# Kernel tuning notes

Hardware: AMD Instinct MI355X
Metric: run time of the kernel (lower is better)

Reference implementation:

```python
import jax, jax.numpy as jnp
import numpy as np

N = 4096
TOPK = 16
LEAKY = 0.2
LN_EPS = 1e-5


def _gat(x, W, a_s, a_d, b, src, dst, heads):
    # PyG-style GATConv (self-loops already included in src/dst).
    n = x.shape[0]
    h = (x @ W).reshape(n, heads, -1)                      # [N,H,F]
    e = jax.nn.leaky_relu((h * a_s).sum(-1)[src] + (h * a_d).sum(-1)[dst], LEAKY)  # [E,H]
    m = jax.ops.segment_max(e, dst, num_segments=n)        # segment softmax over dst
    p = jnp.exp(e - m[dst])
    s = jax.ops.segment_sum(p, dst, num_segments=n)
    alpha = p / s[dst]                                     # [E,H]
    out = jax.ops.segment_sum(alpha[:, :, None] * h[src], dst, num_segments=n)  # [N,H,F]
    return out.reshape(n, -1) + b


def _ln(x, g, b):
    mu = x.mean(-1, keepdims=True)
    v = ((x - mu) ** 2).mean(-1, keepdims=True)
    return (x - mu) / jnp.sqrt(v + LN_EPS) * g + b


def _transformer_layer(x, wqkv, bqkv, wo, bo, g1, b1g, w1, bb1, w2, bb2, g2, b2g, nhead):
    n, d = x.shape
    dh = d // nhead
    qkv = x @ wqkv.T + bqkv                                # [N,3d]
    q, k, v = jnp.split(qkv, 3, axis=-1)
    q = q.reshape(n, nhead, dh)
    k = k.reshape(n, nhead, dh)
    v = v.reshape(n, nhead, dh)
    scores = jnp.einsum('nhd,mhd->hnm', q, k) / jnp.sqrt(jnp.float32(dh))
    attn = jax.nn.softmax(scores, axis=-1)
    o = jnp.einsum('hnm,mhd->nhd', attn, v).reshape(n, d)
    x = _ln(x + (o @ wo.T + bo), g1, b1g)
    ff = jax.nn.relu(x @ w1 + bb1) @ w2 + bb2
    return _ln(x + ff, g2, b2g)


def _learn_graph(window, gl_w, gl_b):
    h = jnp.tanh(window @ gl_w + gl_b)                     # [N,hid]
    sim = h @ h.T                                          # [N,N]
    adj = jax.nn.relu(sim)
    masked = jnp.where(jnp.eye(N, dtype=bool), -1e9, adj)  # exclude self in top-k
    _, idx = jax.lax.top_k(masked, TOPK)                   # [N,TOPK]
    src = idx.reshape(-1)
    dst = jnp.repeat(jnp.arange(N), TOPK)
    loop = jnp.arange(N)
    return jnp.concatenate([src, loop]), jnp.concatenate([dst, loop])


def setup_inputs() -> dict:
    key = jax.random.key(0)
    ks = iter(jax.random.split(key, 64))
    def rn(shape, s=0.05):
        return jax.random.normal(next(ks), shape, jnp.float32) * s
    d = dict(
        window=rn((N, 256), 1.0),
        gl_w=rn((256, 256)), gl_b=rn((256,)),
        enc_W=rn((3, 256, 256)), enc_asrc=rn((3, 4, 64)), enc_adst=rn((3, 4, 64)), enc_b=rn((3, 256)),
        tr_wqkv=rn((2, 768, 256)), tr_bqkv=rn((2, 768)),
        tr_wo=rn((2, 256, 256)), tr_bo=rn((2, 256)),
        tr_ln1_g=jnp.ones((2, 256), jnp.float32), tr_ln1_b=jnp.zeros((2, 256), jnp.float32),
        tr_w1=rn((2, 256, 512)), tr_b1=rn((2, 512)),
        tr_w2=rn((2, 512, 256)), tr_b2=rn((2, 256)),
        tr_ln2_g=jnp.ones((2, 256), jnp.float32), tr_ln2_b=jnp.zeros((2, 256), jnp.float32),
        skip_w=rn((256, 256)), skip_b=rn((256,)),
        dec_W=rn((2, 256, 256)), dec_asrc=rn((2, 4, 64)), dec_adst=rn((2, 4, 64)), dec_b=rn((2, 256)),
        dec_lW=rn((256, 256)), dec_lasrc=rn((1, 1, 256)), dec_ladst=rn((1, 1, 256)), dec_lb=rn((256,)),
    )
    return d


def reference(window, gl_w, gl_b, enc_W, enc_asrc, enc_adst, enc_b,
              tr_wqkv, tr_bqkv, tr_wo, tr_bo, tr_ln1_g, tr_ln1_b,
              tr_w1, tr_b1, tr_w2, tr_b2, tr_ln2_g, tr_ln2_b,
              skip_w, skip_b, dec_W, dec_asrc, dec_adst, dec_b,
              dec_lW, dec_lasrc, dec_ladst, dec_lb):
    src, dst = _learn_graph(window, gl_w, gl_b)
    # encoder: 3 GAT layers with ReLU
    x = window
    for i in range(3):
        x = jax.nn.relu(_gat(x, enc_W[i], enc_asrc[i], enc_adst[i], enc_b[i], src, dst, 4))
    # transformer bottleneck (batch of 1 sequence of N tokens)
    h = x
    for i in range(2):
        h = _transformer_layer(h, tr_wqkv[i], tr_bqkv[i], tr_wo[i], tr_bo[i],
                               tr_ln1_g[i], tr_ln1_b[i], tr_w1[i], tr_b1[i],
                               tr_w2[i], tr_b2[i], tr_ln2_g[i], tr_ln2_b[i], 4)
    # skip connection
    h = h + (window @ skip_w + skip_b)
    # decoder: 2 GAT layers with ReLU, then single-head GAT
    x = h
    for i in range(2):
        x = jax.nn.relu(_gat(x, dec_W[i], dec_asrc[i], dec_adst[i], dec_b[i], src, dst, 4))
    out = _gat(x, dec_lW, dec_lasrc[0], dec_ladst[0], dec_lb, src, dst, 1)
    return out.T
```

## Files before the change

kernel.cpp:

```cpp
#include <hip/hip_runtime.h>
#include <math.h>

#define NN 4096
#define DM 256

enum { ACT_NONE = 0, ACT_RELU = 1, ACT_TANH = 2 };

typedef __attribute__((ext_vector_type(8))) short short8v;
typedef __attribute__((ext_vector_type(16))) float f32x16;

__device__ __forceinline__ unsigned short f2bf(float f) {
  unsigned int u = __float_as_uint(f);
  unsigned int r = (u + 0x7FFFu + ((u >> 16) & 1u)) >> 16;
  return (unsigned short)r;
}
__device__ __forceinline__ float bf2f(unsigned short u) {
  return __uint_as_float(((unsigned int)u) << 16);
}

struct CastJob { const float* s; unsigned short* d; int n4; };
__global__ __launch_bounds__(256) void castall_k(CastJob j0, CastJob j1, CastJob j2) {
  const CastJob* jp = (blockIdx.y == 0) ? &j0 : (blockIdx.y == 1) ? &j1 : &j2;
  const int i = blockIdx.x * 256 + threadIdx.x;
  if (i < jp->n4) {
    const float4 v = ((const float4*)jp->s)[i];
    ushort4 u;
    u.x = f2bf(v.x); u.y = f2bf(v.y); u.z = f2bf(v.z); u.w = f2bf(v.w);
    ((ushort4*)jp->d)[i] = u;
  }
}

struct TJob { const float* s; unsigned short* d; int K; int N; };
struct TJobs { TJob j[11]; };
__global__ __launch_bounds__(256) void tcastall_k(TJobs js) {
  const TJob jb = js.j[blockIdx.z];
  const int n0 = blockIdx.x * 32, k0 = blockIdx.y * 32;
  if (n0 >= jb.N || k0 >= jb.K) return;
  __shared__ float tile[32][33];
  const int tx = threadIdx.x & 31, ty = threadIdx.x >> 5;
#pragma unroll
  for (int r2 = 0; r2 < 4; r2++)
    tile[ty + r2 * 8][tx] = jb.s[(size_t)(k0 + ty + r2 * 8) * jb.N + n0 + tx];
  __syncthreads();
#pragma unroll
  for (int r2 = 0; r2 < 4; r2++)
    jb.d[(size_t)(n0 + ty + r2 * 8) * jb.K + k0 + tx] = f2bf(tile[tx][ty + r2 * 8]);
}

__global__ __launch_bounds__(256) void split_k(
    const float* __restrict__ h, unsigned short* __restrict__ Aext,
    unsigned short* __restrict__ Bext) {
  const int n = blockIdx.x, t = threadIdx.x;
  const float v = h[(size_t)n * DM + t];
  const unsigned short hi = f2bf(v);
  const unsigned short lo = f2bf(v - bf2f(hi));
  unsigned short* ar = Aext + (size_t)n * 768;
  unsigned short* br = Bext + (size_t)n * 768;
  ar[t] = hi; ar[256 + t] = lo; ar[512 + t] = hi;
  br[t] = hi; br[256 + t] = hi; br[512 + t] = lo;
}

template<bool BT, int ACT, bool BIAS, bool RES>
__global__ __launch_bounds__(256) void gemm_k(
    const float* __restrict__ A, const float* __restrict__ B,
    const float* __restrict__ bias, const float* __restrict__ res,
    float* __restrict__ C, int M, int N, int K) {
  __shared__ float As[16][64];
  __shared__ float Bs[16][64];
  const int t = threadIdx.x;
  const int tx = t & 15, ty = t >> 4;
  const int m0 = blockIdx.y * 64, n0 = blockIdx.x * 64;
  float acc[4][4];
#pragma unroll
  for (int i = 0; i < 4; i++)
#pragma unroll
    for (int j = 0; j < 4; j++) acc[i][j] = 0.f;

  const int i_ld = t >> 2, kq = t & 3;
  for (int k0 = 0; k0 < K; k0 += 16) {
    float4 a4 = *(const float4*)(A + (size_t)(m0 + i_ld) * K + k0 + kq * 4);
    As[kq * 4 + 0][i_ld] = a4.x; As[kq * 4 + 1][i_ld] = a4.y;
    As[kq * 4 + 2][i_ld] = a4.z; As[kq * 4 + 3][i_ld] = a4.w;
    if (BT) {
      float4 b4 = *(const float4*)(B + (size_t)(n0 + i_ld) * K + k0 + kq * 4);
      Bs[kq * 4 + 0][i_ld] = b4.x; Bs[kq * 4 + 1][i_ld] = b4.y;
      Bs[kq * 4 + 2][i_ld] = b4.z; Bs[kq * 4 + 3][i_ld] = b4.w;
    } else {
      const int kk = t >> 4, j4 = (t & 15) * 4;
      float4 b4 = *(const float4*)(B + (size_t)(k0 + kk) * N + n0 + j4);
      *(float4*)&Bs[kk][j4] = b4;
    }
    __syncthreads();
#pragma unroll
    for (int kk = 0; kk < 16; kk++) {
      const float4 av = *(const float4*)&As[kk][ty * 4];
      const float4 bv = *(const float4*)&Bs[kk][tx * 4];
      acc[0][0] += av.x * bv.x; acc[0][1] += av.x * bv.y;
      acc[0][2] += av.x * bv.z; acc[0][3] += av.x * bv.w;
      acc[1][0] += av.y * bv.x; acc[1][1] += av.y * bv.y;
      acc[1][2] += av.y * bv.z; acc[1][3] += av.y * bv.w;
      acc[2][0] += av.z * bv.x; acc[2][1] += av.z * bv.y;
      acc[2][2] += av.z * bv.z; acc[2][3] += av.z * bv.w;
      acc[3][0] += av.w * bv.x; acc[3][1] += av.w * bv.y;
      acc[3][2] += av.w * bv.z; acc[3][3] += av.w * bv.w;
    }
    __syncthreads();
  }
  const int n = n0 + tx * 4;
#pragma unroll
  for (int i = 0; i < 4; i++) {
    const int m = m0 + ty * 4 + i;
    float4 v = make_float4(acc[i][0], acc[i][1], acc[i][2], acc[i][3]);
    if (BIAS) {
      v.x += bias[n + 0]; v.y += bias[n + 1];
      v.z += bias[n + 2]; v.w += bias[n + 3];
    }
    if (RES) {
      const float4 rv = *(const float4*)(res + (size_t)m * N + n);
      v.x += rv.x; v.y += rv.y; v.z += rv.z; v.w += rv.w;
    }
    if (ACT == ACT_RELU) {
      v.x = fmaxf(v.x, 0.f); v.y = fmaxf(v.y, 0.f);
      v.z = fmaxf(v.z, 0.f); v.w = fmaxf(v.w, 0.f);
    } else if (ACT == ACT_TANH) {
      v.x = tanhf(v.x); v.y = tanhf(v.y); v.z = tanhf(v.z); v.w = tanhf(v.w);
    }
    *(float4*)(C + (size_t)m * N + n) = v;
  }
}

template<int ACT, bool BIAS, bool RES, bool F32OUT, bool B16OUT>
__global__ __launch_bounds__(256) void mgemm_k(
    const unsigned short* __restrict__ A, const unsigned short* __restrict__ Bt,
    const float* __restrict__ bias, const float* __restrict__ res,
    float* __restrict__ C, unsigned short* __restrict__ Cb,
    int M, int N, int K) {
  __shared__ short As[64][64];
  __shared__ short Bs[64][64];
  const int t = threadIdx.x;
  const int m0 = blockIdx.y * 64, n0 = blockIdx.x * 64;
  const int wid = t >> 6, l = t & 63, l31 = l & 31, g = l >> 5;
  const int wm = wid >> 1, wn = wid & 1;
  f32x16 acc;
#pragma unroll
  for (int r = 0; r < 16; r++) acc[r] = 0.f;

  const int r0 = wid * 16;
  const int lrow = l >> 3;
  const int pos = l & 7;
  const int swz = (pos ^ lrow) << 3;

  for (int k0 = 0; k0 < K; k0 += 64) {
#pragma unroll
    for (int j = 0; j < 2; j++) {
      const int row = r0 + j * 8 + lrow;
      const short* ga = (const short*)A + (size_t)(m0 + row) * K + k0 + swz;
      const short* gb = (const short*)Bt + (size_t)(n0 + row) * K + k0 + swz;
      __builtin_amdgcn_global_load_lds(
          (const __attribute__((address_space(1))) unsigned int*)ga,
          (__attribute__((address_space(3))) unsigned int*)&As[r0 + j * 8][0],
          16, 0, 0);
      __builtin_amdgcn_global_load_lds(
          (const __attribute__((address_space(1))) unsigned int*)gb,
          (__attribute__((address_space(3))) unsigned int*)&Bs[r0 + j * 8][0],
          16, 0, 0);
    }
    __syncthreads();
#pragma unroll
    for (int ck = 0; ck < 4; ck++) {
      const int c = ck * 2 + g;
      const short8v af = *(const short8v*)&As[wm * 32 + l31][(c ^ (l31 & 7)) * 8];
      const short8v bf = *(const short8v*)&Bs[wn * 32 + l31][(c ^ (l31 & 7)) * 8];
      acc = __builtin_amdgcn_mfma_f32_32x32x16_bf16(bf, af, acc, 0, 0, 0);
    }
    __syncthreads();
  }
  const int m = m0 + wm * 32 + l31;
#pragma unroll
  for (int b = 0; b < 4; b++) {
    const int n = n0 + wn * 32 + b * 8 + g * 4;
    float4 v = make_float4(acc[b * 4 + 0], acc[b * 4 + 1],
                           acc[b * 4 + 2], acc[b * 4 + 3]);
    if (BIAS) {
      v.x += bias[n + 0]; v.y += bias[n + 1];
      v.z += bias[n + 2]; v.w += bias[n + 3];
    }
    if (RES) {
      const float4 rv = *(const float4*)(res + (size_t)m * N + n);
      v.x += rv.x; v.y += rv.y; v.z += rv.z; v.w += rv.w;
    }
    if (ACT == ACT_RELU) {
      v.x = fmaxf(v.x, 0.f); v.y = fmaxf(v.y, 0.f);
      v.z = fmaxf(v.z, 0.f); v.w = fmaxf(v.w, 0.f);
    }
    if (F32OUT) *(float4*)(C + (size_t)m * N + n) = v;
    if (B16OUT) {
      ushort4 uv;
      uv.x = f2bf(v.x); uv.y = f2bf(v.y); uv.z = f2bf(v.z); uv.w = f2bf(v.w);
      *(ushort4*)(Cb + (size_t)m * N + n) = uv;
    }
  }
}

__global__ __launch_bounds__(256) void topk16_k(
    const float* __restrict__ sim, int* __restrict__ idxo, int rowbase) {
  const int r = blockIdx.x, t = threadIdx.x;
  const int grow = rowbase + r;
  float val[16];
#pragma unroll
  for (int q = 0; q < 16; q++) {
    const int jj = q * 256 + t;
    float v = sim[(size_t)r * NN + jj];
    v = fmaxf(v, 0.f);
    if (jj == grow) v = -1.f;
    val[q] = v;
  }
  __shared__ float cv[64];
  __shared__ int cjs[64];
  const int wave = t >> 6, lane = t & 63;
  float myv = -3.f; int myj = 0;
  for (int it = 0; it < 16; it++) {
    float bv = -10.f; int bj = 0;
#pragma unroll
    for (int q = 0; q < 16; q++)
      if (val[q] > bv) { bv = val[q]; bj = q * 256 + t; }
#pragma unroll
    for (int off = 1; off < 64; off <<= 1) {
      const float ov = __shfl_xor(bv, off);
      const int oj = __shfl_xor(bj, off);
      if (ov > bv || (ov == bv && oj < bj)) { bv = ov; bj = oj; }
    }
    if (lane == it) { myv = bv; myj = bj; }
    if ((bj & 255) == t) {
      const int q = bj >> 8;
#pragma unroll
      for (int qq = 0; qq < 16; qq++) if (qq == q) val[qq] = -2.f;
    }
  }
  if (lane < 16) { cv[wave * 16 + lane] = myv; cjs[wave * 16 + lane] = myj; }
  __syncthreads();
  if (wave == 0) {
    float bv2 = cv[lane]; int bj2 = cjs[lane];
    for (int it = 0; it < 16; it++) {
      float wv = bv2; int wj = bj2;
#pragma unroll
      for (int off = 1; off < 64; off <<= 1) {
        const float ov = __shfl_xor(wv, off);
        const int oj = __shfl_xor(wj, off);
        if (ov > wv || (ov == wv && oj < wj)) { wv = ov; wj = oj; }
      }
      if (lane == 0) idxo[(size_t)grow * 16 + it] = wj;
      if (wj == bj2) bv2 = -3.f;
    }
  }
}

template<int H>
__global__ __launch_bounds__(256) void gat_prep_k(
    const float* __restrict__ h, const float* __restrict__ as,
    const float* __restrict__ ad, float* __restrict__ es, float* __restrict__ ed) {
  __shared__ float bs[4], bd[4];
  const int n = blockIdx.x, t = threadIdx.x;
  const float v = h[(size_t)n * DM + t];
  float ps = v * as[t];
  float pd = v * ad[t];
#pragma unroll
  for (int off = 32; off >= 1; off >>= 1) {
    ps += __shfl_down(ps, off, 64);
    pd += __shfl_down(pd, off, 64);
  }
  const int wave = t >> 6, lane = t & 63;
  if (H == 4) {
    if (lane == 0) { es[n * 4 + wave] = ps; ed[n * 4 + wave] = pd; }
  } else {
    if (lane == 0) { bs[wave] = ps; bd[wave] = pd; }
    __syncthreads();
    if (t == 0) {
      es[n] = bs[0] + bs[1] + bs[2] + bs[3];
      ed[n] = bd[0] + bd[1] + bd[2] + bd[3];
    }
  }
}

template<int H, bool RELU, bool B16OUT>
__global__ __launch_bounds__(256) void gat_aggr_k(
    const float* __restrict__ h, const float* __restrict__ es,
    const float* __restrict__ ed, const int* __restrict__ idx,
    const float* __restrict__ bias, float* __restrict__ out,
    unsigned short* __restrict__ outb) {
  const int j = blockIdx.x, t = threadIdx.x;
  const int hd = (H == 4) ? (t >> 6) : 0;
  __shared__ int srcs[17];
  if (t < 16) srcs[t] = idx[(size_t)j * 16 + t];
  if (t == 16) srcs[16] = j;
  __syncthreads();
  const float edj = ed[j * H + hd];
  float e[17]; float m = -1e30f;
#pragma unroll
  for (int k = 0; k < 17; k++) {
    float ev = es[srcs[k] * H + hd] + edj;
    ev = (ev >= 0.f) ? ev : 0.2f * ev;
    e[k] = ev; m = fmaxf(m, ev);
  }
  float s = 0.f;
#pragma unroll
  for (int k = 0; k < 17; k++) { e[k] = expf(e[k] - m); s += e[k]; }
  const float inv = 1.f / s;
  float acc = 0.f;
#pragma unroll
  for (int k = 0; k < 17; k++) acc += e[k] * h[(size_t)srcs[k] * DM + t];
  acc = acc * inv + bias[t];
  if (RELU) acc = fmaxf(acc, 0.f);
  out[(size_t)j * DM + t] = acc;
  if (B16OUT) outb[(size_t)j * DM + t] = f2bf(acc);
}

__global__ __launch_bounds__(256) void kvfrag_k(
    const short* __restrict__ qkvs, short* __restrict__ kf,
    short* __restrict__ vf) {
  const int kc = blockIdx.x;
  const int h = blockIdx.y;
  const int t = threadIdx.x;
  __shared__ short Ks[32][72];
  __shared__ short Vs[32][72];
  {
    const int row = t >> 3, ch = t & 7;
    const short* kp = qkvs + (size_t)(kc * 32 + row) * 768 + 256 + h * 64 + ch * 8;
    *(short8v*)&Ks[row][ch * 8] = *(const short8v*)kp;
    const short* vp = qkvs + (size_t)(kc * 32 + row) * 768 + 512 + h * 64 + ch * 8;
    *(short8v*)&Vs[row][ch * 8] = *(const short8v*)vp;
  }
  __syncthreads();
  {
    const int dc = t >> 6, l = t & 63, l31 = l & 31, g = l >> 5;
    short8v kv;
#pragma unroll
    for (int e = 0; e < 8; e++) kv[e] = Ks[l31][dc * 16 + g * 8 + e];
    *(short8v*)(kf + ((size_t)(h * 128 + kc) * 4 + dc) * 512 + l * 8) = kv;
  }
  {
    const int db = t >> 7, kg = (t >> 6) & 1, l = t & 63, l31 = l & 31, g = l >> 5;
    short8v vv;
#pragma unroll
    for (int e = 0; e < 8; e++) {
      const int j = kg * 16 + g * 8 + e;
      const int jp = (j & 19) | ((j & 4) << 1) | ((j & 8) >> 1);
      vv[e] = Vs[jp][db * 32 + l31];
    }
    *(short8v*)(vf + (((size_t)(h * 128 + kc) * 2 + db) * 2 + kg) * 512 + l * 8) = vv;
  }
}

#define LOADKV(KF, VF, KC) do {                                               \
    const short* kp_ = kfrag + ((size_t)(KC)) * 2048 + l * 8;                 \
    KF##0 = *(const short8v*)(kp_);                                           \
    KF##1 = *(const short8v*)(kp_ + 512);                                     \
    KF##2 = *(const short8v*)(kp_ + 1024);                                    \
    KF##3 = *(const short8v*)(kp_ + 1536);                                    \
    const short* vp_ = vfrag + ((size_t)(KC)) * 2048 + l * 8;                 \
    VF##0 = *(const short8v*)(vp_);                                           \
    VF##1 = *(const short8v*)(vp_ + 512);                                     \
    VF##2 = *(const short8v*)(vp_ + 1024);                                    \
    VF##3 = *(const short8v*)(vp_ + 1536);                                    \
  } while (0)

#define PROCESS(KF, VF) do {                                                  \
    f32x16 accS;                                                              \
    _Pragma("unroll") for (int r = 0; r < 16; r++) accS[r] = 0.f;             \
    __builtin_amdgcn_s_setprio(1);                                            \
    accS = __builtin_amdgcn_mfma_f32_32x32x16_bf16(KF##0, qf[0], accS, 0, 0, 0); \
    accS = __builtin_amdgcn_mfma_f32_32x32x16_bf16(KF##1, qf[1], accS, 0, 0, 0); \
    accS = __builtin_amdgcn_mfma_f32_32x32x16_bf16(KF##2, qf[2], accS, 0, 0, 0); \
    accS = __builtin_amdgcn_mfma_f32_32x32x16_bf16(KF##3, qf[3], accS, 0, 0, 0); \
    __builtin_amdgcn_s_setprio(0);                                            \
    float mt = -1e30f;                                                        \
    _Pragma("unroll") for (int r = 0; r < 16; r++) mt = fmaxf(mt, accS[r]);   \
    mt = fmaxf(mt, __shfl_xor(mt, 32));                                       \
    float pv[16]; float ls = 0.f;                                             \
    if (__all(mt <= mrun + 11.5416f)) {                                       \
      _Pragma("unroll") for (int r = 0; r < 16; r++) {                        \
        pv[r] = exp2f(accS[r] - mrun); ls += pv[r];                           \
      }                                                                       \
      ls += __shfl_xor(ls, 32); lrun += ls;                                   \
    } else {                                                                  \
      const float mnew = fmaxf(mrun, mt);                                     \
      const float corr = exp2f(mrun - mnew);                                  \
      _Pragma("unroll") for (int r = 0; r < 16; r++) {                        \
        pv[r] = exp2f(accS[r] - mnew); ls += pv[r];                           \
      }                                                                       \
      ls += __shfl_xor(ls, 32);                                               \
      lrun = lrun * corr + ls; mrun = mnew;                                   \
      _Pragma("unroll") for (int r = 0; r < 16; r++) {                        \
        accO[0][r] *= corr; accO[1][r] *= corr;                               \
      }                                                                       \
    }                                                                         \
    union { unsigned int u[8]; short8v s[2]; } pf;                            \
    _Pragma("unroll") for (int r = 0; r < 8; r++) {                           \
      unsigned int po;                                                        \
      asm("v_cvt_pk_bf16_f32 %0, %1, %2"                                      \
          : "=v"(po) : "v"(pv[2 * r]), "v"(pv[2 * r + 1]));                   \
      pf.u[r] = po;                                                           \
    }                                                                         \
    __builtin_amdgcn_s_setprio(1);                                            \
    accO[0] = __builtin_amdgcn_mfma_f32_32x32x16_bf16(VF##0, pf.s[0], accO[0], 0, 0, 0); \
    accO[0] = __builtin_amdgcn_mfma_f32_32x32x16_bf16(VF##1, pf.s[1], accO[0], 0, 0, 0); \
    accO[1] = __builtin_amdgcn_mfma_f32_32x32x16_bf16(VF##2, pf.s[0], accO[1], 0, 0, 0); \
    accO[1] = __builtin_amdgcn_mfma_f32_32x32x16_bf16(VF##3, pf.s[1], accO[1], 0, 0, 0); \
    __builtin_amdgcn_s_setprio(0);                                            \
  } while (0)

__global__ __launch_bounds__(256) void attn_flash_k(
    const short* __restrict__ qkvs, const short* __restrict__ kfb,
    const short* __restrict__ vfb, unsigned short* __restrict__ opart,
    float* __restrict__ ml) {
  const int t = threadIdx.x;
  const int wv = t >> 6;
  const int l = t & 63;
  const int qb = (blockIdx.x * 4 + wv) * 32;
  const int h = blockIdx.y;
  const int z = blockIdx.z;
  const int l31 = l & 31, g = l >> 5;

  short8v qf[4];
  {
    const short* qp = qkvs + (size_t)(qb + l31) * 768 + h * 64 + g * 8;
#pragma unroll
    for (int c = 0; c < 4; c++) {
      short8v qv = *(const short8v*)(qp + c * 16);
#pragma unroll
      for (int e = 0; e < 8; e++)
        qv[e] = (short)f2bf(bf2f((unsigned short)qv[e]) * 0.18033688f);
      qf[c] = qv;
    }
  }

  f32x16 accO[2];
#pragma unroll
  for (int r = 0; r < 16; r++) { accO[0][r] = 0.f; accO[1][r] = 0.f; }
  float mrun = -1e30f, lrun = 0.f;

  const short* kfrag = kfb + (size_t)h * 128 * 2048;
  const short* vfrag = vfb + (size_t)h * 128 * 2048;
  const int kc0 = z * 32;

  short8v kA0, kA1, kA2, kA3, vA0, vA1, vA2, vA3;
  short8v kB0, kB1, kB2, kB3, vB0, vB1, vB2, vB3;
  LOADKV(kA, vA, kc0);
  for (int it = 0; it < 16; it++) {
    LOADKV(kB, vB, kc0 + (it * 2 + 1));
    PROCESS(kA, vA);
    LOADKV(kA, vA, kc0 + ((it * 2 + 2) & 31));
    PROCESS(kB, vB);
  }

  const int q = qb + l31;
  unsigned short* op = opart + ((size_t)z * NN + q) * DM + h * 64;
#pragma unroll
  for (int db = 0; db < 2; db++) {
#pragma unroll
    for (int rq = 0; rq < 4; rq++) {
      ushort4 v4;
      v4.x = f2bf(accO[db][rq * 4 + 0]);
      v4.y = f2bf(accO[db][rq * 4 + 1]);
      v4.z = f2bf(accO[db][rq * 4 + 2]);
      v4.w = f2bf(accO[db][rq * 4 + 3]);
      *(ushort4*)(op + db * 32 + rq * 8 + g * 4) = v4;
    }
  }
  if (g == 0) {
    ml[(((size_t)z * 4 + h) * NN + q) * 2 + 0] = mrun;
    ml[(((size_t)z * 4 + h) * NN + q) * 2 + 1] = lrun;
  }
}

__global__ __launch_bounds__(256) void attn_merge_k(
    const unsigned short* __restrict__ opart, const float* __restrict__ ml,
    unsigned short* __restrict__ ob) {
  const int q = blockIdx.x;
  const int t = threadIdx.x;
  const int h = t >> 6;
  float m[4], lv[4];
#pragma unroll
  for (int z = 0; z < 4; z++) {
    m[z]  = ml[(((size_t)z * 4 + h) * NN + q) * 2 + 0];
    lv[z] = ml[(((size_t)z * 4 + h) * NN + q) * 2 + 1];
  }
  const float ms = fmaxf(fmaxf(m[0], m[1]), fmaxf(m[2], m[3]));
  float w[4]; float ls = 0.f;
#pragma unroll
  for (int z = 0; z < 4; z++) {
    w[z] = exp2f(m[z] - ms);
    ls += lv[z] * w[z];
  }
  const float inv = 1.f / ls;
  float acc = 0.f;
#pragma unroll
  for (int z = 0; z < 4; z++)
    acc += bf2f(opart[((size_t)z * NN + q) * DM + t]) * w[z];
  ob[(size_t)q * DM + t] = f2bf(acc * inv);
}

__global__ __launch_bounds__(256) void ln_k(
    const float* __restrict__ x, const float* __restrict__ g,
    const float* __restrict__ b, float* __restrict__ y,
    unsigned short* __restrict__ yb) {
  __shared__ float bs[4], bs2[4];
  const int n = blockIdx.x, t = threadIdx.x;
  const float v = x[(size_t)n * DM + t];
  float s = v, s2 = v * v;
#pragma unroll
  for (int off = 32; off >= 1; off >>= 1) {
    s += __shfl_down(s, off, 64);
    s2 += __shfl_down(s2, off, 64);
  }
  const int wave = t >> 6, lane = t & 63;
  if (lane == 0) { bs[wave] = s; bs2[wave] = s2; }
  __syncthreads();
  const float ts = bs[0] + bs[1] + bs[2] + bs[3];
  const float ts2 = bs2[0] + bs2[1] + bs2[2] + bs2[3];
  const float mu = ts * (1.f / 256.f);
  const float var = ts2 * (1.f / 256.f) - mu * mu;
  const float rstd = 1.f / sqrtf(var + 1e-5f);
  const float o = (v - mu) * rstd * g[t] + b[t];
  y[(size_t)n * DM + t] = o;
  yb[(size_t)n * DM + t] = f2bf(o);
}

__global__ __launch_bounds__(1024) void transpose_k(
    const float* __restrict__ x, float* __restrict__ out) {
  __shared__ float tile[32][33];
  const int n0 = blockIdx.x * 32, c0 = blockIdx.y * 32;
  const int tx = threadIdx.x, ty = threadIdx.y;
  tile[ty][tx] = x[(size_t)(n0 + ty) * DM + c0 + tx];
  __syncthreads();
  out[(size_t)(c0 + ty) * NN + n0 + tx] = tile[tx][ty];
}

extern "C" void kernel_launch(void* const* d_in, const int* in_sizes, int n_in,
                              void* d_out, int out_size, void* d_ws, size_t ws_size,
                              hipStream_t stream) {
  (void)in_sizes; (void)n_in; (void)out_size; (void)ws_size;
  const float* window   = (const float*)d_in[0];
  const float* gl_w     = (const float*)d_in[1];
  const float* gl_b     = (const float*)d_in[2];
  const float* enc_W    = (const float*)d_in[3];
  const float* enc_asrc = (const float*)d_in[4];
  const float* enc_adst = (const float*)d_in[5];
  const float* enc_b    = (const float*)d_in[6];
  const float* tr_wqkv  = (const float*)d_in[7];
  const float* tr_bqkv  = (const float*)d_in[8];
  const float* tr_wo    = (const float*)d_in[9];
  const float* tr_bo    = (const float*)d_in[10];
  const float* tr_ln1_g = (const float*)d_in[11];
  const float* tr_ln1_b = (const float*)d_in[12];
  const float* tr_w1    = (const float*)d_in[13];
  const float* tr_b1    = (const float*)d_in[14];
  const float* tr_w2    = (const float*)d_in[15];
  const float* tr_b2    = (const float*)d_in[16];
  const float* tr_ln2_g = (const float*)d_in[17];
  const float* tr_ln2_b = (const float*)d_in[18];
  const float* skip_w   = (const float*)d_in[19];
  const float* skip_b   = (const float*)d_in[20];
  const float* dec_W    = (const float*)d_in[21];
  const float* dec_asrc = (const float*)d_in[22];
  const float* dec_adst = (const float*)d_in[23];
  const float* dec_b    = (const float*)d_in[24];
  const float* dec_lW   = (const float*)d_in[25];
  const float* dec_lasrc= (const float*)d_in[26];
  const float* dec_ladst= (const float*)d_in[27];
  const float* dec_lb   = (const float*)d_in[28];
  float* outp = (float*)d_out;

  float* ws   = (float*)d_ws;
  float* xa   = ws;
  float* xb   = ws + 1048576;
  float* hp   = ws + 2097152;
  float* t1   = ws + 3145728;
  float* hgl  = t1;
  float* mlb  = t1;
  float* qkvb = ws + 4194304;
  float* Rg   = ws + 6291456;
  float* simc = Rg;
  unsigned short* opartb = (unsigned short*)Rg;
  unsigned short* ffb    = (unsigned short*)Rg;
  float* es   = ws + 8388608;
  float* ed   = ws + 8404992;
  int*   idx  = (int*)(ws + 8421376);
  unsigned short* winb = (unsigned short*)(ws + 8486912);
  unsigned short* actb = (unsigned short*)(ws + 9011200);
  unsigned short* wb   = (unsigned short*)(ws + 9535488);

  unsigned short* encWt = wb;
  unsigned short* wqkvb = wb + 196608;
  unsigned short* wob   = wb + 589824;
  unsigned short* w1t   = wb + 720896;
  unsigned short* w2t   = wb + 983040;
  unsigned short* skipt = wb + 1245184;
  unsigned short* dect  = wb + 1310720;
  unsigned short* declt = wb + 1441792;

  unsigned short* Aext = (unsigned short*)qkvb;
  unsigned short* Bext = (unsigned short*)xa;

  short* kfb = (short*)hp;
  short* vfb = (short*)hp + 1048576;

  const dim3 B256(256);

  {
    CastJob c0{window, winb, 262144};
    CastJob c1{tr_wqkv, wqkvb, 98304};
    CastJob c2{tr_wo, wob, 32768};
    castall_k<<<dim3(1024, 3), B256, 0, stream>>>(c0, c1, c2);
    TJobs tj;
    for (int i = 0; i < 3; i++) tj.j[i] = {enc_W + (size_t)i * 65536, encWt + (size_t)i * 65536, 256, 256};
    for (int i = 0; i < 2; i++) tj.j[3 + i] = {tr_w1 + (size_t)i * 131072, w1t + (size_t)i * 131072, 256, 512};
    for (int i = 0; i < 2; i++) tj.j[5 + i] = {tr_w2 + (size_t)i * 131072, w2t + (size_t)i * 131072, 512, 256};
    tj.j[7] = {skip_w, skipt, 256, 256};
    for (int i = 0; i < 2; i++) tj.j[8 + i] = {dec_W + (size_t)i * 65536, dect + (size_t)i * 65536, 256, 256};
    tj.j[10] = {dec_lW, declt, 256, 256};
    tcastall_k<<<dim3(16, 16, 11), B256, 0, stream>>>(tj);
  }

  gemm_k<false, ACT_TANH, true, false><<<dim3(DM / 64, NN / 64), B256, 0, stream>>>(
      window, gl_w, gl_b, nullptr, hgl, NN, DM, DM);

  split_k<<<dim3(NN), B256, 0, stream>>>(hgl, Aext, Bext);
  for (int c = 0; c < 8; c++) {
    mgemm_k<ACT_NONE, false, false, true, false><<<dim3(64, 8), B256, 0, stream>>>(
        Aext + (size_t)c * 512 * 768, Bext, nullptr, nullptr, simc, nullptr,
        512, NN, 768);
    topk16_k<<<dim3(512), B256, 0, stream>>>(simc, idx, c * 512);
  }

  for (int i = 0; i < 3; i++) {
    const unsigned short* ain = (i == 0) ? winb : actb;
    mgemm_k<ACT_NONE, false, false, true, false><<<dim3(4, 64), B256, 0, stream>>>(
        ain, encWt + (size_t)i * 65536, nullptr, nullptr, hp, nullptr, NN, DM, DM);
    gat_prep_k<4><<<dim3(NN), B256, 0, stream>>>(hp, enc_asrc + i * 256, enc_adst + i * 256, es, ed);
    gat_aggr_k<4, true, true><<<dim3(NN), B256, 0, stream>>>(
        hp, es, ed, idx, enc_b + i * 256, xa, actb);
  }

  for (int i = 0; i < 2; i++) {
    mgemm_k<ACT_NONE, true, false, false, true><<<dim3(12, 64), B256, 0, stream>>>(
        actb, wqkvb + (size_t)i * 196608, tr_bqkv + i * 768, nullptr,
        nullptr, (unsigned short*)qkvb, NN, 768, DM);
    kvfrag_k<<<dim3(128, 4), B256, 0, stream>>>((const short*)qkvb, kfb, vfb);
    attn_flash_k<<<dim3(NN / 128, 4, 4), B256, 0, stream>>>(
        (const short*)qkvb, kfb, vfb, opartb, mlb);
    attn_merge_k<<<dim3(NN), B256, 0, stream>>>(opartb, mlb, actb);
    mgemm_k<ACT_NONE, true, true, true, false><<<dim3(4, 64), B256, 0, stream>>>(
        actb, wob + (size_t)i * 65536, tr_bo + i * 256, xa, t1, nullptr, NN, DM, DM);
    ln_k<<<dim3(NN), B256, 0, stream>>>(t1, tr_ln1_g + i * 256, tr_ln1_b + i * 256, xb, actb);
    mgemm_k<ACT_RELU, true, false, false, true><<<dim3(8, 64), B256, 0, stream>>>(
        actb, w1t + (size_t)i * 131072, tr_b1 + i * 512, nullptr,
        nullptr, ffb, NN, 512, DM);
    mgemm_k<ACT_NONE, true, true, true, false><<<dim3(4, 64), B256, 0, stream>>>(
        ffb, w2t + (size_t)i * 131072, tr_b2 + i * 256, xb, t1, nullptr, NN, DM, 512);
    ln_k<<<dim3(NN), B256, 0, stream>>>(t1, tr_ln2_g + i * 256, tr_ln2_b + i * 256, xa, actb);
  }

  mgemm_k<ACT_NONE, true, true, false, true><<<dim3(4, 64), B256, 0, stream>>>(
      winb, skipt, skip_b, xa, nullptr, actb, NN, DM, DM);

  mgemm_k<ACT_NONE, false, false, true, false><<<dim3(4, 64), B256, 0, stream>>>(
      actb, dect, nullptr, nullptr, hp, nullptr, NN, DM, DM);
  gat_prep_k<4><<<dim3(NN), B256, 0, stream>>>(hp, dec_asrc, dec_adst, es, ed);
  gat_aggr_k<4, true, true><<<dim3(NN), B256, 0, stream>>>(hp, es, ed, idx, dec_b, xb, actb);

  mgemm_k<ACT_NONE, false, false, true, false><<<dim3(4, 64), B256, 0, stream>>>(
      actb, dect + 65536, nullptr, nullptr, hp, nullptr, NN, DM, DM);
  gat_prep_k<4><<<dim3(NN), B256, 0, stream>>>(hp, dec_asrc + 256, dec_adst + 256, es, ed);
  gat_aggr_k<4, true, true><<<dim3(NN), B256, 0, stream>>>(hp, es, ed, idx, dec_b + 256, xb, actb);

  mgemm_k<ACT_NONE, false, false, true, false><<<dim3(4, 64), B256, 0, stream>>>(
      actb, declt, nullptr, nullptr, hp, nullptr, NN, DM, DM);
  gat_prep_k<1><<<dim3(NN), B256, 0, stream>>>(hp, dec_lasrc, dec_ladst, es, ed);
  gat_aggr_k<1, false, false><<<dim3(NN), B256, 0, stream>>>(hp, es, ed, idx, dec_lb, xa, nullptr);

  transpose_k<<<dim3(NN / 32, DM / 32), dim3(32, 32), 0, stream>>>(xa, outp);
}
```

Baseline: 693.9 us.

## Move graph-learning GEMM to split-bf16 MFMA and fuse tanh with hi/lo split

The fp32 SIMT GEMM for tanh(window@gl_w+b) is replaced by a split-bf16 (hi/lo, 3-term) MFMA GEMM. Its epilogue applies bias and tanh and writes the extended hi/lo operands for the similarity GEMM directly, which removes the separate split kernel and the fp32 intermediate round trip. The similarity GEMM also moves to a new kernel with 64x128 tiles and two accumulators per wave, so A fragments are reused across more columns. The cost is extra split/transpose kernels on window and gl_w, and a precision change in the tanh input from fp32 to a 3-term bf16 emulation.

```diff
diff --git a/kernel.cpp b/kernel.cpp
--- a/kernel.cpp
+++ b/kernel.cpp
@@ -47,85 +47,33 @@
     jb.d[(size_t)(n0 + ty + r2 * 8) * jb.K + k0 + tx] = f2bf(tile[tx][ty + r2 * 8]);
 }
 
-__global__ __launch_bounds__(256) void split_k(
-    const float* __restrict__ h, unsigned short* __restrict__ Aext,
-    unsigned short* __restrict__ Bext) {
+__global__ __launch_bounds__(256) void wsplit_k(
+    const float* __restrict__ w, unsigned short* __restrict__ Awin) {
   const int n = blockIdx.x, t = threadIdx.x;
-  const float v = h[(size_t)n * DM + t];
+  const float v = w[(size_t)n * DM + t];
   const unsigned short hi = f2bf(v);
   const unsigned short lo = f2bf(v - bf2f(hi));
-  unsigned short* ar = Aext + (size_t)n * 768;
-  unsigned short* br = Bext + (size_t)n * 768;
+  unsigned short* ar = Awin + (size_t)n * 768;
   ar[t] = hi; ar[256 + t] = lo; ar[512 + t] = hi;
-  br[t] = hi; br[256 + t] = hi; br[512 + t] = lo;
-}
-
-template<bool BT, int ACT, bool BIAS, bool RES>
-__global__ __launch_bounds__(256) void gemm_k(
-    const float* __restrict__ A, const float* __restrict__ B,
-    const float* __restrict__ bias, const float* __restrict__ res,
-    float* __restrict__ C, int M, int N, int K) {
-  __shared__ float As[16][64];
-  __shared__ float Bs[16][64];
-  const int t = threadIdx.x;
-  const int tx = t & 15, ty = t >> 4;
-  const int m0 = blockIdx.y * 64, n0 = blockIdx.x * 64;
-  float acc[4][4];
-#pragma unroll
-  for (int i = 0; i < 4; i++)
-#pragma unroll
-    for (int j = 0; j < 4; j++) acc[i][j] = 0.f;
-
-  const int i_ld = t >> 2, kq = t & 3;
-  for (int k0 = 0; k0 < K; k0 += 16) {
-    float4 a4 = *(const float4*)(A + (size_t)(m0 + i_ld) * K + k0 + kq * 4);
-    As[kq * 4 + 0][i_ld] = a4.x; As[kq * 4 + 1][i_ld] = a4.y;
-    As[kq * 4 + 2][i_ld] = a4.z; As[kq * 4 + 3][i_ld] = a4.w;
-    if (BT) {
-      float4 b4 = *(const float4*)(B + (size_t)(n0 + i_ld) * K + k0 + kq * 4);
-      Bs[kq * 4 + 0][i_ld] = b4.x; Bs[kq * 4 + 1][i_ld] = b4.y;
-      Bs[kq * 4 + 2][i_ld] = b4.z; Bs[kq * 4 + 3][i_ld] = b4.w;
-    } else {
-      const int kk = t >> 4, j4 = (t & 15) * 4;
-      float4 b4 = *(const float4*)(B + (size_t)(k0 + kk) * N + n0 + j4);
-      *(float4*)&Bs[kk][j4] = b4;
-    }
-    __syncthreads();
-#pragma unroll
-    for (int kk = 0; kk < 16; kk++) {
-      const float4 av = *(const float4*)&As[kk][ty * 4];
-      const float4 bv = *(const float4*)&Bs[kk][tx * 4];
-      acc[0][0] += av.x * bv.x; acc[0][1] += av.x * bv.y;
-      acc[0][2] += av.x * bv.z; acc[0][3] += av.x * bv.w;
-      acc[1][0] += av.y * bv.x; acc[1][1] += av.y * bv.y;
-      acc[1][2] += av.y * bv.z; acc[1][3] += av.y * bv.w;
-      acc[2][0] += av.z * bv.x; acc[2][1] += av.z * bv.y;
-      acc[2][2] += av.z * bv.z; acc[2][3] += av.z * bv.w;
-      acc[3][0] += av.w * bv.x; acc[3][1] += av.w * bv.y;
-      acc[3][2] += av.w * bv.z; acc[3][3] += av.w * bv.w;
-    }
-    __syncthreads();
-  }
-  const int n = n0 + tx * 4;
-#pragma unroll
-  for (int i = 0; i < 4; i++) {
-    const int m = m0 + ty * 4 + i;
-    float4 v = make_float4(acc[i][0], acc[i][1], acc[i][2], acc[i][3]);
-    if (BIAS) {
-      v.x += bias[n + 0]; v.y += bias[n + 1];
-      v.z += bias[n + 2]; v.w += bias[n + 3];
-    }
-    if (RES) {
-      const float4 rv = *(const float4*)(res + (size_t)m * N + n);
-      v.x += rv.x; v.y += rv.y; v.z += rv.z; v.w += rv.w;
-    }
-    if (ACT == ACT_RELU) {
-      v.x = fmaxf(v.x, 0.f); v.y = fmaxf(v.y, 0.f);
-      v.z = fmaxf(v.z, 0.f); v.w = fmaxf(v.w, 0.f);
-    } else if (ACT == ACT_TANH) {
-      v.x = tanhf(v.x); v.y = tanhf(v.y); v.z = tanhf(v.z); v.w = tanhf(v.w);
-    }
-    *(float4*)(C + (size_t)m * N + n) = v;
+}
+
+__global__ __launch_bounds__(256) void gsplit_k(
+    const float* __restrict__ g, unsigned short* __restrict__ Bgl) {
+  __shared__ float tile[32][33];
+  const int d0 = blockIdx.x * 32, k0 = blockIdx.y * 32;
+  const int tx = threadIdx.x & 31, ty = threadIdx.x >> 5;
+#pragma unroll
+  for (int r2 = 0; r2 < 4; r2++)
+    tile[ty + r2 * 8][tx] = g[(size_t)(k0 + ty + r2 * 8) * DM + d0 + tx];
+  __syncthreads();
+#pragma unroll
+  for (int r2 = 0; r2 < 4; r2++) {
+    const int d = d0 + ty + r2 * 8, k = k0 + tx;
+    const float v = tile[tx][ty + r2 * 8];
+    const unsigned short hi = f2bf(v);
+    const unsigned short lo = f2bf(v - bf2f(hi));
+    unsigned short* br = Bgl + (size_t)d * 768;
+    br[k] = hi; br[256 + k] = hi; br[512 + k] = lo;
   }
 }
 
@@ -199,6 +147,134 @@
       uv.x = f2bf(v.x); uv.y = f2bf(v.y); uv.z = f2bf(v.z); uv.w = f2bf(v.w);
       *(ushort4*)(Cb + (size_t)m * N + n) = uv;
     }
+  }
+}
+
+__global__ __launch_bounds__(256) void mgemm_ts_k(
+    const unsigned short* __restrict__ A, const unsigned short* __restrict__ Bt,
+    const float* __restrict__ bias, unsigned short* __restrict__ Aext,
+    unsigned short* __restrict__ Bext, int M, int N, int K) {
+  __shared__ short As[64][64];
+  __shared__ short Bs[64][64];
+  const int t = threadIdx.x;
+  const int m0 = blockIdx.y * 64, n0 = blockIdx.x * 64;
+  const int wid = t >> 6, l = t & 63, l31 = l & 31, g = l >> 5;
+  const int wm = wid >> 1, wn = wid & 1;
+  f32x16 acc;
+#pragma unroll
+  for (int r = 0; r < 16; r++) acc[r] = 0.f;
+
+  const int r0 = wid * 16;
+  const int lrow = l >> 3;
+  const int pos = l & 7;
+  const int swz = (pos ^ lrow) << 3;
+
+  for (int k0 = 0; k0 < K; k0 += 64) {
+#pragma unroll
+    for (int j = 0; j < 2; j++) {
+      const int row = r0 + j * 8 + lrow;
+      const short* ga = (const short*)A + (size_t)(m0 + row) * K + k0 + swz;
+      const short* gb = (const short*)Bt + (size_t)(n0 + row) * K + k0 + swz;
+      __builtin_amdgcn_global_load_lds(
+          (const __attribute__((address_space(1))) unsigned int*)ga,
+          (__attribute__((address_space(3))) unsigned int*)&As[r0 + j * 8][0],
+          16, 0, 0);
+      __builtin_amdgcn_global_load_lds(
+          (const __attribute__((address_space(1))) unsigned int*)gb,
+          (__attribute__((address_space(3))) unsigned int*)&Bs[r0 + j * 8][0],
+          16, 0, 0);
+    }
+    __syncthreads();
+#pragma unroll
+    for (int ck = 0; ck < 4; ck++) {
+      const int c = ck * 2 + g;
+      const short8v af = *(const short8v*)&As[wm * 32 + l31][(c ^ (l31 & 7)) * 8];
+      const short8v bf = *(const short8v*)&Bs[wn * 32 + l31][(c ^ (l31 & 7)) * 8];
+      acc = __builtin_amdgcn_mfma_f32_32x32x16_bf16(bf, af, acc, 0, 0, 0);
+    }
+    __syncthreads();
+  }
+  const int m = m0 + wm * 32 + l31;
+  unsigned short* ar = Aext + (size_t)m * 768;
+  unsigned short* br = Bext + (size_t)m * 768;
+#pragma unroll
+  for (int b = 0; b < 4; b++) {
+    const int n = n0 + wn * 32 + b * 8 + g * 4;
+    ushort4 hi4, lo4;
+#pragma unroll
+    for (int e = 0; e < 4; e++) {
+      float v = acc[b * 4 + e] + bias[n + e];
+      v = tanhf(v);
+      const unsigned short hi = f2bf(v);
+      const unsigned short lo = f2bf(v - bf2f(hi));
+      ((unsigned short*)&hi4)[e] = hi;
+      ((unsigned short*)&lo4)[e] = lo;
+    }
+    *(ushort4*)(ar + n) = hi4;
+    *(ushort4*)(ar + 256 + n) = lo4;
+    *(ushort4*)(ar + 512 + n) = hi4;
+    *(ushort4*)(br + n) = hi4;
+    *(ushort4*)(br + 256 + n) = hi4;
+    *(ushort4*)(br + 512 + n) = lo4;
+  }
+}
+
+__global__ __launch_bounds__(256) void mgemm2_k(
+    const unsigned short* __restrict__ A, const unsigned short* __restrict__ Bt,
+    float* __restrict__ C, int M, int N, int K) {
+  __shared__ short As[64][64];
+  __shared__ short Bs[128][64];
+  const int t = threadIdx.x;
+  const int m0 = blockIdx.y * 64, n0 = blockIdx.x * 128;
+  const int wid = t >> 6, l = t & 63, l31 = l & 31, g = l >> 5;
+  const int wm = wid >> 1, wn = wid & 1;
+  f32x16 acc0, acc1;
+#pragma unroll
+  for (int r = 0; r < 16; r++) { acc0[r] = 0.f; acc1[r] = 0.f; }
+
+  const int lrow = l >> 3;
+  const int pos = l & 7;
+  const int swz = (pos ^ lrow) << 3;
+
+  for (int k0 = 0; k0 < K; k0 += 64) {
+#pragma unroll
+    for (int j = 0; j < 2; j++) {
+      const int row = wid * 16 + j * 8 + lrow;
+      const short* ga = (const short*)A + (size_t)(m0 + row) * K + k0 + swz;
+      __builtin_amdgcn_global_load_lds(
+          (const __attribute__((address_space(1))) unsigned int*)ga,
+          (__attribute__((address_space(3))) unsigned int*)&As[wid * 16 + j * 8][0],
+          16, 0, 0);
+    }
+#pragma unroll
+    for (int j = 0; j < 4; j++) {
+      const int row = wid * 32 + j * 8 + lrow;
+      const short* gb = (const short*)Bt + (size_t)(n0 + row) * K + k0 + swz;
+      __builtin_amdgcn_global_load_lds(
+          (const __attribute__((address_space(1))) unsigned int*)gb,
+          (__attribute__((address_space(3))) unsigned int*)&Bs[wid * 32 + j * 8][0],
+          16, 0, 0);
+    }
+    __syncthreads();
+#pragma unroll
+    for (int ck = 0; ck < 4; ck++) {
+      const int c = ck * 2 + g;
+      const short8v af = *(const short8v*)&As[wm * 32 + l31][(c ^ (l31 & 7)) * 8];
+      const short8v bf0 = *(const short8v*)&Bs[wn * 64 + l31][(c ^ (l31 & 7)) * 8];
+      const short8v bf1 = *(const short8v*)&Bs[wn * 64 + 32 + l31][(c ^ (l31 & 7)) * 8];
+      acc0 = __builtin_amdgcn_mfma_f32_32x32x16_bf16(bf0, af, acc0, 0, 0, 0);
+      acc1 = __builtin_amdgcn_mfma_f32_32x32x16_bf16(bf1, af, acc1, 0, 0, 0);
+    }
+    __syncthreads();
+  }
+  const int m = m0 + wm * 32 + l31;
+#pragma unroll
+  for (int b = 0; b < 4; b++) {
+    const int n = n0 + wn * 64 + b * 8 + g * 4;
+    *(float4*)(C + (size_t)m * N + n) =
+        make_float4(acc0[b * 4 + 0], acc0[b * 4 + 1], acc0[b * 4 + 2], acc0[b * 4 + 3]);
+    *(float4*)(C + (size_t)m * N + n + 32) =
+        make_float4(acc1[b * 4 + 0], acc1[b * 4 + 1], acc1[b * 4 + 2], acc1[b * 4 + 3]);
   }
 }
 
@@ -576,7 +652,6 @@
   float* xb   = ws + 1048576;
   float* hp   = ws + 2097152;
   float* t1   = ws + 3145728;
-  float* hgl  = t1;
   float* mlb  = t1;
   float* qkvb = ws + 4194304;
   float* Rg   = ws + 6291456;
@@ -601,6 +676,8 @@
 
   unsigned short* Aext = (unsigned short*)qkvb;
   unsigned short* Bext = (unsigned short*)xa;
+  unsigned short* AwinExt = (unsigned short*)Rg;
+  unsigned short* BglExt  = actb;
 
   short* kfb = (short*)hp;
   short* vfb = (short*)hp + 1048576;
@@ -622,14 +699,14 @@
     tcastall_k<<<dim3(16, 16, 11), B256, 0, stream>>>(tj);
   }
 
-  gemm_k<false, ACT_TANH, true, false><<<dim3(DM / 64, NN / 64), B256, 0, stream>>>(
-      window, gl_w, gl_b, nullptr, hgl, NN, DM, DM);
-
-  split_k<<<dim3(NN), B256, 0, stream>>>(hgl, Aext, Bext);
+  wsplit_k<<<dim3(NN), B256, 0, stream>>>(window, AwinExt);
+  gsplit_k<<<dim3(8, 8), B256, 0, stream>>>(gl_w, BglExt);
+  mgemm_ts_k<<<dim3(4, 64), B256, 0, stream>>>(
+      AwinExt, BglExt, gl_b, Aext, Bext, NN, DM, 768);
+
   for (int c = 0; c < 8; c++) {
-    mgemm_k<ACT_NONE, false, false, true, false><<<dim3(64, 8), B256, 0, stream>>>(
-        Aext + (size_t)c * 512 * 768, Bext, nullptr, nullptr, simc, nullptr,
-        512, NN, 768);
+    mgemm2_k<<<dim3(32, 8), B256, 0, stream>>>(
+        Aext + (size_t)c * 512 * 768, Bext, simc, 512, NN, 768);
     topk16_k<<<dim3(512), B256, 0, stream>>>(simc, idx, c * 512);
   }
 
```

Result: slower. 711.4 us (+2.5%).
